# Optimization experiments

Hardware: AMD Instinct MI355X
Metric: run time of the kernel (lower is better)

The kernel has to match this reference:

```python
import jax, jax.numpy as jnp
import numpy as np

B, S, IN_DIM, EMBED, HEADS, WINDOW = 2, 2048, 1024, 1024, 16, 256
HEAD_DIM = EMBED // HEADS
NEG_FILL = -9.0e15


def setup_inputs() -> dict:
    key = jax.random.key(0)
    k1, k2, k3, k4 = jax.random.split(key, 4)
    x = jax.random.normal(k1, (B, S, IN_DIM), dtype=jnp.float32)
    # padding_mask: positions with value 1 get zeroed in q/k/v (matches masked_fill semantics)
    padding_mask = jax.random.randint(k2, (B, S), 0, 2, dtype=jnp.int32)
    # xavier-uniform-like init scale for the linear weights
    lim_qkv = np.sqrt(6.0 / (IN_DIM + 3 * EMBED)).astype(np.float32)
    lim_o = np.sqrt(6.0 / (EMBED + EMBED)).astype(np.float32)
    Wqkv = jax.random.uniform(k3, (3 * EMBED, IN_DIM), jnp.float32, -lim_qkv, lim_qkv)
    bqkv = jnp.zeros((3 * EMBED,), jnp.float32)
    Wo = jax.random.uniform(k4, (EMBED, EMBED), jnp.float32, -lim_o, lim_o)
    bo = jnp.zeros((EMBED,), jnp.float32)
    return {"x": x, "padding_mask": padding_mask, "Wqkv": Wqkv, "bqkv": bqkv, "Wo": Wo, "bo": bo}


def reference(x, padding_mask, Wqkv, bqkv, Wo, bo):
    b, s, _ = x.shape
    h, hd, pad = HEADS, HEAD_DIM, WINDOW // 2
    # qkv projection: torch Linear is x @ W.T + b
    qkv = x @ Wqkv.T + bqkv                      # [B, S, 3E]
    qkv = qkv.reshape(b, s, h, 3 * hd).transpose(0, 2, 1, 3)  # [B, H, S, 3*hd]
    q, k, v = jnp.split(qkv, 3, axis=-1)          # each [B, H, S, hd]
    # zero out padded positions in q, k, v where padding_mask == 1
    pm = (padding_mask != 0)[:, None, :, None]    # [B, 1, S, 1]
    q = jnp.where(pm, 0.0, q)
    k = jnp.where(pm, 0.0, k)
    v = jnp.where(pm, 0.0, v)
    # dense banded scores: identical math to the unfold-based band compute
    scores = jnp.einsum("bhsd,bhtd->bhst", q, k)  # [B, H, S, S]
    idx = jnp.arange(s)
    band = jnp.abs(idx[None, :] - idx[:, None]) <= pad  # |i-j| <= window/2
    scores = jnp.where(band, scores, jnp.float32(NEG_FILL))
    scores = scores / jnp.sqrt(jnp.float32(hd))   # original scales AFTER the fill
    attn = jax.nn.softmax(scores, axis=-1)        # [B, H, S, S]
    vals = jnp.einsum("bhst,bhtd->bhsd", attn, v)  # [B, H, S, hd]
    vals = vals.transpose(0, 2, 1, 3).reshape(b, s, h * hd)  # [B, S, E]
    return vals @ Wo.T + bo
```

## Files before the change

### kernel.cpp

```cpp
#include <hip/hip_runtime.h>
#include <stdint.h>

#define S_LEN 2048
#define EMBED 1024
#define HEADS 16
#define HD 64
#define M_ROWS 4096
#define N_QKV 3072
#define KDIM 1024
#define SP 2336
#define CLP2 200

typedef __attribute__((ext_vector_type(8))) short short8;
typedef __attribute__((ext_vector_type(4))) float f32x4;

__device__ __forceinline__ unsigned short f2bf(float f) {
  union { float f; uint32_t u; } c; c.f = f;
  uint32_t u = c.u;
  u += 0x7fffu + ((u >> 16) & 1u);
  return (unsigned short)(u >> 16);
}

__device__ __forceinline__ void gload_lds16(const unsigned short* g, unsigned short* l) {
  __builtin_amdgcn_global_load_lds(
      (const __attribute__((address_space(1))) void*)g,
      (__attribute__((address_space(3))) void*)l, 16, 0, 0);
}

#define XQ 1048576
#define WQKVQ 786432
#define WOQ 262144
#define CVTQ (XQ + WQKVQ + WOQ)
__global__ __launch_bounds__(256) void cvt3_kernel(
    const float* __restrict__ x, const float* __restrict__ wqkv, const float* __restrict__ wo,
    unsigned short* __restrict__ xb, unsigned short* __restrict__ wqkvb, unsigned short* __restrict__ wob,
    unsigned short* __restrict__ vTp) {
  int i = blockIdx.x * blockDim.x + threadIdx.x;
  if (i < CVTQ) {
    const float* s; unsigned short* d; int off;
    if (i < XQ)               { s = x;    d = xb;    off = i; }
    else if (i < XQ + WQKVQ)  { s = wqkv; d = wqkvb; off = i - XQ; }
    else                      { s = wo;   d = wob;   off = i - XQ - WQKVQ; }
    float4 f = reinterpret_cast<const float4*>(s)[off];
    ushort4 o;
    o.x = f2bf(f.x); o.y = f2bf(f.y); o.z = f2bf(f.z); o.w = f2bf(f.w);
    reinterpret_cast<ushort4*>(d)[off] = o;
  } else {
    int j = i - CVTQ;
    int row = j / 72, p = j % 72;
    int off = row * 584 + (p < 32 ? p : 544 + (p - 32));
    reinterpret_cast<ushort4*>(vTp)[off] = (ushort4){0, 0, 0, 0};
  }
}

__global__ __launch_bounds__(256) void gemm_qkv(
    const unsigned short* __restrict__ A, const unsigned short* __restrict__ Bm,
    const float* __restrict__ bias, const int* __restrict__ pm,
    unsigned short* __restrict__ qo, unsigned short* __restrict__ ko,
    unsigned short* __restrict__ vTp)
{
  __shared__ __align__(16) unsigned short smem[16384];
  unsigned short* As = smem;
  unsigned short* Bs = smem + 4096;
  const int t = threadIdx.x, wave = t >> 6, lane = t & 63;
  const int m16 = lane & 15, q4 = lane >> 4;
  const int wm = wave >> 1, wn = wave & 1;
  const int bid = blockIdx.x;
  const int mb = bid >> 4, nb = bid & 15;
  const int srow = lane >> 2, scol = (lane & 3) << 3;
  const unsigned short* pA = A + (size_t)(mb * 64 + wave * 16 + srow) * KDIM + scol;
  const unsigned short* pB0 = Bm + (size_t)(nb * 192 + wave * 48 + srow) * KDIM + scol;
  const unsigned short* pB1 = Bm + (size_t)(nb * 192 + wave * 48 + 16 + srow) * KDIM + scol;
  const unsigned short* pB2 = Bm + (size_t)(nb * 192 + wave * 48 + 32 + srow) * KDIM + scol;
  f32x4 acc[2][6];
#pragma unroll
  for (int i_ = 0; i_ < 2; i_++)
#pragma unroll
    for (int j_ = 0; j_ < 6; j_++) acc[i_][j_] = (f32x4){0.f, 0.f, 0.f, 0.f};

  for (int kt = 0; kt < KDIM; kt += 64) {
    __syncthreads();
#pragma unroll
    for (int h = 0; h < 2; h++) {
      gload_lds16(pA + kt + h * 32,  As + h * 2048 + (wave * 16) * 32);
      gload_lds16(pB0 + kt + h * 32, Bs + h * 6144 + (wave * 48) * 32);
      gload_lds16(pB1 + kt + h * 32, Bs + h * 6144 + (wave * 48 + 16) * 32);
      gload_lds16(pB2 + kt + h * 32, Bs + h * 6144 + (wave * 48 + 32) * 32);
    }
    __syncthreads();
#pragma unroll
    for (int h = 0; h < 2; h++) {
      short8 af[2], bf[6];
#pragma unroll
      for (int mt = 0; mt < 2; mt++)
        af[mt] = *reinterpret_cast<const short8*>(&As[h * 2048 + (wm * 32 + mt * 16 + m16) * 32 + q4 * 8]);
#pragma unroll
      for (int nt = 0; nt < 6; nt++)
        bf[nt] = *reinterpret_cast<const short8*>(&Bs[h * 6144 + (wn * 96 + nt * 16 + m16) * 32 + q4 * 8]);
#pragma unroll
      for (int mt = 0; mt < 2; mt++)
#pragma unroll
        for (int nt = 0; nt < 6; nt++)
          acc[mt][nt] = __builtin_amdgcn_mfma_f32_16x16x32_bf16(af[mt], bf[nt], acc[mt][nt], 0, 0, 0);
    }
  }

  __syncthreads();
  float pmv[2][4];
#pragma unroll
  for (int mt = 0; mt < 2; mt++)
#pragma unroll
    for (int reg = 0; reg < 4; reg++) {
      int row = mb * 64 + wm * 32 + mt * 16 + q4 * 4 + reg;
      pmv[mt][reg] = (pm[row] != 0) ? 0.0f : 1.0f;
    }
#pragma unroll
  for (int nt = 0; nt < 6; nt++) {
    int cloc = wn * 96 + nt * 16 + m16;
    float bv = bias[nb * 192 + cloc];
#pragma unroll
    for (int mt = 0; mt < 2; mt++) {
#pragma unroll
      for (int reg = 0; reg < 4; reg++) {
        int rloc = wm * 32 + mt * 16 + q4 * 4 + reg;
        smem[rloc * CLP2 + cloc] = f2bf((acc[mt][nt][reg] + bv) * pmv[mt][reg]);
      }
    }
  }
  __syncthreads();
  const int s0 = mb * 64;
  const int bh = (s0 >> 11) * 16 + nb, s0l = s0 & 2047;
  {
    int r = t >> 2, seg = t & 3;
    const unsigned short* sq = &smem[r * CLP2 + seg * 16];
    unsigned short* dq = qo + ((size_t)(bh * 2048 + s0l + r)) * 64 + seg * 16;
    *reinterpret_cast<short8*>(dq)     = *reinterpret_cast<const short8*>(sq);
    *reinterpret_cast<short8*>(dq + 8) = *reinterpret_cast<const short8*>(sq + 8);
    const unsigned short* sk = &smem[r * CLP2 + 64 + seg * 16];
    unsigned short* dk = ko + ((size_t)(bh * 2048 + s0l + r)) * 64 + seg * 16;
    *reinterpret_cast<short8*>(dk)     = *reinterpret_cast<const short8*>(sk);
    *reinterpret_cast<short8*>(dk + 8) = *reinterpret_cast<const short8*>(sk + 8);
  }
  {
    int d = t & 63, qtr = t >> 6;
    short8 tmp0, tmp1;
#pragma unroll
    for (int jj = 0; jj < 8; jj++) {
      tmp0[jj] = (short)smem[(qtr * 16 + jj) * CLP2 + 128 + d];
      tmp1[jj] = (short)smem[(qtr * 16 + 8 + jj) * CLP2 + 128 + d];
    }
    unsigned short* dst = vTp + (size_t)(bh * 64 + d) * SP + 128 + s0l + qtr * 16;
    *reinterpret_cast<short8*>(dst)     = tmp0;
    *reinterpret_cast<short8*>(dst + 8) = tmp1;
  }
}

__global__ __launch_bounds__(256) void gemm_out(
    const unsigned short* __restrict__ A, const unsigned short* __restrict__ Bm,
    const float* __restrict__ bias, float* __restrict__ out)
{
  __shared__ __align__(16) unsigned char smemraw[17408];
  unsigned short* As = (unsigned short*)smemraw;
  unsigned short* Bs = As + 4096;
  float* Cldf = (float*)smemraw;
  const int t = threadIdx.x, wave = t >> 6, lane = t & 63;
  const int m16 = lane & 15, q4 = lane >> 4;
  const int wm = wave >> 1, wn = wave & 1;
  const int flat = blockIdx.y * 16 + blockIdx.x;
  const int xcd = flat & 7, bi = flat >> 3;
  const int mb = xcd * 8 + (bi & 7);
  const int nb = bi >> 3;
  const int srow = lane >> 2, scol = (lane & 3) << 3;
  const unsigned short* pA = A + (size_t)(mb * 64 + wave * 16 + srow) * KDIM + scol;
  const unsigned short* pB = Bm + (size_t)(nb * 64 + wave * 16 + srow) * KDIM + scol;
  f32x4 acc[2][2];
#pragma unroll
  for (int i_ = 0; i_ < 2; i_++)
#pragma unroll
    for (int j_ = 0; j_ < 2; j_++) acc[i_][j_] = (f32x4){0.f, 0.f, 0.f, 0.f};
  for (int kt = 0; kt < KDIM; kt += 64) {
    __syncthreads();
#pragma unroll
    for (int h = 0; h < 2; h++) {
      gload_lds16(pA + kt + h * 32, As + h * 2048 + (wave * 16) * 32);
      gload_lds16(pB + kt + h * 32, Bs + h * 2048 + (wave * 16) * 32);
    }
    __syncthreads();
#pragma unroll
    for (int h = 0; h < 2; h++) {
      short8 af[2], bf[2];
#pragma unroll
      for (int mt = 0; mt < 2; mt++)
        af[mt] = *reinterpret_cast<const short8*>(&As[h * 2048 + (wm * 32 + mt * 16 + m16) * 32 + q4 * 8]);
#pragma unroll
      for (int nt = 0; nt < 2; nt++)
        bf[nt] = *reinterpret_cast<const short8*>(&Bs[h * 2048 + (wn * 32 + nt * 16 + m16) * 32 + q4 * 8]);
#pragma unroll
      for (int mt = 0; mt < 2; mt++)
#pragma unroll
        for (int nt = 0; nt < 2; nt++)
          acc[mt][nt] = __builtin_amdgcn_mfma_f32_16x16x32_bf16(af[mt], bf[nt], acc[mt][nt], 0, 0, 0);
    }
  }
  __syncthreads();
#pragma unroll
  for (int nt = 0; nt < 2; nt++) {
    int cloc = wn * 32 + nt * 16 + m16;
    float bv = bias[nb * 64 + cloc];
#pragma unroll
    for (int mt = 0; mt < 2; mt++) {
#pragma unroll
      for (int reg = 0; reg < 4; reg++) {
        int rloc = wm * 32 + mt * 16 + q4 * 4 + reg;
        Cldf[rloc * 68 + cloc] = acc[mt][nt][reg] + bv;
      }
    }
  }
  __syncthreads();
  {
    int r = t >> 2, seg = t & 3;
    float* dst = out + (size_t)(mb * 64 + r) * EMBED + nb * 64 + seg * 16;
    const float* srcl = &Cldf[r * 68 + seg * 16];
#pragma unroll
    for (int j = 0; j < 4; j++)
      *reinterpret_cast<float4*>(dst + j * 4) = *reinterpret_cast<const float4*>(srcl + j * 4);
  }
}

__global__ __launch_bounds__(256, 4) void attn_kernel(
    const unsigned short* __restrict__ q, const unsigned short* __restrict__ k,
    const unsigned short* __restrict__ vTp, unsigned short* __restrict__ vals)
{
  __shared__ __align__(16) unsigned short Pld[4][16][296];
  const int bid = blockIdx.x;
  const int bh = bid & 31, qtg = bid >> 5;
  const int lane = threadIdx.x & 63, wave = threadIdx.x >> 6;
  const int qt = qtg * 4 + wave;
  const int i0 = qt * 16, w0 = i0 - 128;
  const int m16 = lane & 15, q4 = lane >> 4;

  const unsigned short* qb = q + ((size_t)(bh * 2048 + i0 + m16)) * 64 + q4 * 8;
  short8 aq0 = *reinterpret_cast<const short8*>(qb);
  short8 aq1 = *reinterpret_cast<const short8*>(qb + 32);

  float sum[4] = {0.f, 0.f, 0.f, 0.f};
#pragma unroll
  for (int ct = 0; ct < 18; ct++) {
    bool live = (ct < 17) && (w0 + ct * 16 + 15 >= 0) && (w0 + ct * 16 < 2048);
    if (live) {
      int js = w0 + ct * 16 + m16;
      int jc = js < 0 ? 0 : (js > 2047 ? 2047 : js);
      const unsigned short* kb = k + ((size_t)(bh * 2048 + jc)) * 64 + q4 * 8;
      short8 b0 = *reinterpret_cast<const short8*>(kb);
      short8 b1 = *reinterpret_cast<const short8*>(kb + 32);
      f32x4 a = {0.f, 0.f, 0.f, 0.f};
      a = __builtin_amdgcn_mfma_f32_16x16x32_bf16(aq0, b0, a, 0, 0, 0);
      a = __builtin_amdgcn_mfma_f32_16x16x32_bf16(aq1, b1, a, 0, 0, 0);
#pragma unroll
      for (int reg = 0; reg < 4; reg++) {
        int i = i0 + q4 * 4 + reg;
        bool valid = (js >= 0) && (js < 2048) && (js >= i - 128) && (js <= i + 128);
        float e = valid ? __expf(a[reg] * 0.125f) : 0.0f;
        sum[reg] += e;
        Pld[wave][q4 * 4 + reg][ct * 16 + m16] = f2bf(e);
      }
    } else {
#pragma unroll
      for (int reg = 0; reg < 4; reg++)
        Pld[wave][q4 * 4 + reg][ct * 16 + m16] = 0;
    }
  }
  float rden[4];
#pragma unroll
  for (int reg = 0; reg < 4; reg++) {
    float s = sum[reg];
    s += __shfl_xor(s, 1);
    s += __shfl_xor(s, 2);
    s += __shfl_xor(s, 4);
    s += __shfl_xor(s, 8);
    rden[reg] = 1.0f / s;
  }
  __syncthreads();
  short8 ap[9];
#pragma unroll
  for (int kc = 0; kc < 9; kc++)
    ap[kc] = *reinterpret_cast<const short8*>(&Pld[wave][m16][kc * 32 + q4 * 8]);

  const int b = bh >> 4, h = bh & 15;
#pragma unroll
  for (int dt = 0; dt < 4; dt++) {
    f32x4 av = {0.f, 0.f, 0.f, 0.f};
    const unsigned short* vb = vTp + ((size_t)(bh * 64 + dt * 16 + m16)) * SP + i0 + q4 * 8;
#pragma unroll
    for (int kc = 0; kc < 9; kc++) {
      short8 bv = *reinterpret_cast<const short8*>(vb + kc * 32);
      av = __builtin_amdgcn_mfma_f32_16x16x32_bf16(ap[kc], bv, av, 0, 0, 0);
    }
#pragma unroll
    for (int reg = 0; reg < 4; reg++)
      Pld[wave][q4 * 4 + reg][dt * 16 + m16] = f2bf(av[reg] * rden[reg]);
  }
  {
    int srow = lane >> 2, seg = lane & 3;
    unsigned short* dst = vals + ((size_t)(b * 2048 + i0 + srow)) * 1024 + h * 64 + seg * 16;
    const unsigned short* srcl = &Pld[wave][srow][seg * 16];
    *reinterpret_cast<short8*>(dst)     = *reinterpret_cast<const short8*>(srcl);
    *reinterpret_cast<short8*>(dst + 8) = *reinterpret_cast<const short8*>(srcl + 8);
  }
}

extern "C" void kernel_launch(void* const* d_in, const int* in_sizes, int n_in,
                              void* d_out, int out_size, void* d_ws, size_t ws_size,
                              hipStream_t stream) {
  const float* x    = (const float*)d_in[0];
  const int*   pm   = (const int*)d_in[1];
  const float* Wqkv = (const float*)d_in[2];
  const float* bqkv = (const float*)d_in[3];
  const float* Wo   = (const float*)d_in[4];
  const float* bo   = (const float*)d_in[5];
  float* out = (float*)d_out;
  char* ws = (char*)d_ws;

  unsigned short* xb    = (unsigned short*)(ws);
  unsigned short* vals  = (unsigned short*)(ws);
  unsigned short* Wqkvb = (unsigned short*)(ws +  8388608);
  unsigned short* Wob   = (unsigned short*)(ws + 14680064);
  unsigned short* qbuf  = (unsigned short*)(ws + 16777216);
  unsigned short* kbuf  = (unsigned short*)(ws + 25165824);
  unsigned short* vTp   = (unsigned short*)(ws + 33554432);

  cvt3_kernel<<<8768, 256, 0, stream>>>(x, Wqkv, Wo, xb, Wqkvb, Wob, vTp);
  gemm_qkv<<<1024, 256, 0, stream>>>(xb, Wqkvb, bqkv, pm, qbuf, kbuf, vTp);
  attn_kernel<<<1024, 256, 0, stream>>>(qbuf, kbuf, vTp, vals);
  gemm_out<<<dim3(16, 64), 256, 0, stream>>>(vals, Wob, bo, out);
}
```

Baseline: 183.0 us.

## Stage shared K and V window tiles in LDS for attention blocks

The attention kernel now has each 4-wave block cooperatively load a 320-row K window and a 64x320 V^T window into LDS once, using async global-to-LDS loads with XOR swizzling. The four waves then read K and V from LDS instead of each fetching its own overlapping window from global memory. The score probabilities are held in registers until after the barrier, so the K/V buffer can be reused as the P staging area. LDS use grows to 80KB per block and launch bounds drop to 2 blocks per SM, which lowers occupancy in exchange for less redundant global traffic.

```diff
diff --git a/kernel.cpp b/kernel.cpp
--- a/kernel.cpp
+++ b/kernel.cpp
@@ -227,48 +227,70 @@
   }
 }
 
-__global__ __launch_bounds__(256, 4) void attn_kernel(
+__global__ __launch_bounds__(256, 2) void attn_kernel(
     const unsigned short* __restrict__ q, const unsigned short* __restrict__ k,
     const unsigned short* __restrict__ vTp, unsigned short* __restrict__ vals)
 {
-  __shared__ __align__(16) unsigned short Pld[4][16][296];
+  __shared__ __align__(16) unsigned short smem[40960];
+  unsigned short* Ks = smem;
+  unsigned short* Vs = smem + 20480;
+  unsigned short* Pld = smem;
+
   const int bid = blockIdx.x;
-  const int bh = bid & 31, qtg = bid >> 5;
+  const int bh = bid & 31, qg = bid >> 5;
   const int lane = threadIdx.x & 63, wave = threadIdx.x >> 6;
-  const int qt = qtg * 4 + wave;
-  const int i0 = qt * 16, w0 = i0 - 128;
+  const int i0b = qg * 64;
+  const int i0 = i0b + wave * 16;
   const int m16 = lane & 15, q4 = lane >> 4;
+
+  const unsigned short* kbase = k + (size_t)bh * 2048 * 64;
+#pragma unroll
+  for (int n = 0; n < 10; n++) {
+    int idx = (n * 4 + wave) * 64 + lane;
+    int krow = idx >> 3, seg = idx & 7;
+    int grow = i0b - 128 + krow;
+    grow = grow < 0 ? 0 : (grow > 2047 ? 2047 : grow);
+    int lseg = seg ^ (krow & 7);
+    gload_lds16(kbase + (size_t)grow * 64 + lseg * 8, Ks + (n * 4 + wave) * 512);
+  }
+  const unsigned short* vbase = vTp + (size_t)bh * 64 * SP + i0b;
+#pragma unroll
+  for (int n = 0; n < 10; n++) {
+    int idx = (n * 4 + wave) * 64 + lane;
+    int vrow = idx / 40, rem = idx % 40;
+    int l = (rem & ~7) | ((rem & 7) ^ (vrow & 7));
+    gload_lds16(vbase + (size_t)vrow * SP + l * 8, Vs + (n * 4 + wave) * 512);
+  }
 
   const unsigned short* qb = q + ((size_t)(bh * 2048 + i0 + m16)) * 64 + q4 * 8;
   short8 aq0 = *reinterpret_cast<const short8*>(qb);
   short8 aq1 = *reinterpret_cast<const short8*>(qb + 32);
 
+  __syncthreads();
+
   float sum[4] = {0.f, 0.f, 0.f, 0.f};
+  uint32_t pP[18][2];
 #pragma unroll
   for (int ct = 0; ct < 18; ct++) {
-    bool live = (ct < 17) && (w0 + ct * 16 + 15 >= 0) && (w0 + ct * 16 < 2048);
-    if (live) {
-      int js = w0 + ct * 16 + m16;
-      int jc = js < 0 ? 0 : (js > 2047 ? 2047 : js);
-      const unsigned short* kb = k + ((size_t)(bh * 2048 + jc)) * 64 + q4 * 8;
-      short8 b0 = *reinterpret_cast<const short8*>(kb);
-      short8 b1 = *reinterpret_cast<const short8*>(kb + 32);
-      f32x4 a = {0.f, 0.f, 0.f, 0.f};
-      a = __builtin_amdgcn_mfma_f32_16x16x32_bf16(aq0, b0, a, 0, 0, 0);
-      a = __builtin_amdgcn_mfma_f32_16x16x32_bf16(aq1, b1, a, 0, 0, 0);
-#pragma unroll
-      for (int reg = 0; reg < 4; reg++) {
-        int i = i0 + q4 * 4 + reg;
-        bool valid = (js >= 0) && (js < 2048) && (js >= i - 128) && (js <= i + 128);
-        float e = valid ? __expf(a[reg] * 0.125f) : 0.0f;
-        sum[reg] += e;
-        Pld[wave][q4 * 4 + reg][ct * 16 + m16] = f2bf(e);
-      }
-    } else {
-#pragma unroll
-      for (int reg = 0; reg < 4; reg++)
-        Pld[wave][q4 * 4 + reg][ct * 16 + m16] = 0;
-    }
+    int r = (wave + ct) * 16 + m16;
+    int js = i0b - 128 + r;
+    const unsigned short* kr = Ks + r * 64;
+    short8 b0 = *reinterpret_cast<const short8*>(kr + ((q4 ^ (r & 7)) * 8));
+    short8 b1 = *reinterpret_cast<const short8*>(kr + (((q4 + 4) ^ (r & 7)) * 8));
+    f32x4 a = {0.f, 0.f, 0.f, 0.f};
+    a = __builtin_amdgcn_mfma_f32_16x16x32_bf16(aq0, b0, a, 0, 0, 0);
+    a = __builtin_amdgcn_mfma_f32_16x16x32_bf16(aq1, b1, a, 0, 0, 0);
+    unsigned short pe[4];
+#pragma unroll
+    for (int reg = 0; reg < 4; reg++) {
+      int i = i0 + q4 * 4 + reg;
+      bool valid = (js >= 0) && (js < 2048) && (js >= i - 128) && (js <= i + 128);
+      float e = valid ? __expf(a[reg] * 0.125f) : 0.0f;
+      sum[reg] += e;
+      pe[reg] = f2bf(e);
+    }
+    pP[ct][0] = (uint32_t)pe[0] | ((uint32_t)pe[1] << 16);
+    pP[ct][1] = (uint32_t)pe[2] | ((uint32_t)pe[3] << 16);
   }
   float rden[4];
 #pragma unroll
@@ -280,30 +302,44 @@
     s += __shfl_xor(s, 8);
     rden[reg] = 1.0f / s;
   }
-  __syncthreads();
+
+  __syncthreads();
+
+  unsigned short* Pw = Pld + wave * 16 * 296;
+#pragma unroll
+  for (int ct = 0; ct < 18; ct++) {
+    Pw[(q4 * 4 + 0) * 296 + ct * 16 + m16] = (unsigned short)(pP[ct][0] & 0xFFFF);
+    Pw[(q4 * 4 + 1) * 296 + ct * 16 + m16] = (unsigned short)(pP[ct][0] >> 16);
+    Pw[(q4 * 4 + 2) * 296 + ct * 16 + m16] = (unsigned short)(pP[ct][1] & 0xFFFF);
+    Pw[(q4 * 4 + 3) * 296 + ct * 16 + m16] = (unsigned short)(pP[ct][1] >> 16);
+  }
   short8 ap[9];
 #pragma unroll
   for (int kc = 0; kc < 9; kc++)
-    ap[kc] = *reinterpret_cast<const short8*>(&Pld[wave][m16][kc * 32 + q4 * 8]);
+    ap[kc] = *reinterpret_cast<const short8*>(&Pw[m16 * 296 + kc * 32 + q4 * 8]);
 
   const int b = bh >> 4, h = bh & 15;
 #pragma unroll
   for (int dt = 0; dt < 4; dt++) {
+    int vrow = dt * 16 + m16;
+    const unsigned short* vr = Vs + vrow * 320;
     f32x4 av = {0.f, 0.f, 0.f, 0.f};
-    const unsigned short* vb = vTp + ((size_t)(bh * 64 + dt * 16 + m16)) * SP + i0 + q4 * 8;
 #pragma unroll
     for (int kc = 0; kc < 9; kc++) {
-      short8 bv = *reinterpret_cast<const short8*>(vb + kc * 32);
+      int jseg = kc * 4 + wave * 2 + q4;
+      if (jseg > 39) jseg = 39;
+      int sseg = (jseg & ~7) | ((jseg & 7) ^ (vrow & 7));
+      short8 bv = *reinterpret_cast<const short8*>(vr + sseg * 8);
       av = __builtin_amdgcn_mfma_f32_16x16x32_bf16(ap[kc], bv, av, 0, 0, 0);
     }
 #pragma unroll
     for (int reg = 0; reg < 4; reg++)
-      Pld[wave][q4 * 4 + reg][dt * 16 + m16] = f2bf(av[reg] * rden[reg]);
+      Pw[(q4 * 4 + reg) * 296 + dt * 16 + m16] = f2bf(av[reg] * rden[reg]);
   }
   {
     int srow = lane >> 2, seg = lane & 3;
     unsigned short* dst = vals + ((size_t)(b * 2048 + i0 + srow)) * 1024 + h * 64 + seg * 16;
-    const unsigned short* srcl = &Pld[wave][srow][seg * 16];
+    const unsigned short* srcl = &Pw[srow * 296 + seg * 16];
     *reinterpret_cast<short8*>(dst)     = *reinterpret_cast<const short8*>(srcl);
     *reinterpret_cast<short8*>(dst + 8) = *reinterpret_cast<const short8*>(srcl + 8);
   }
```

New measurement: 170.1 us. -7.0%, faster.
